# Performance work log

Hardware: AMD Instinct MI355X
Metric: run time of the kernel (lower is better)

The kernel has to match this reference:

```python
import jax, jax.numpy as jnp
import numpy as np

D = 2048
HQ = 32
HKV = 8
DH = D // HQ          # 64
GROUP = HQ // HKV     # 4
B, T = 2, 2048


def setup_inputs() -> dict:
    key = jax.random.key(0)
    ks = jax.random.split(key, 5)
    s = 0.02
    return {
        "x": jax.random.normal(ks[0], (B, T, D), dtype=jnp.float32),
        "Wq": jax.random.normal(ks[1], (D, D), dtype=jnp.float32) * s,
        "Wk": jax.random.normal(ks[2], (D, HKV * DH), dtype=jnp.float32) * s,
        "Wv": jax.random.normal(ks[3], (D, HKV * DH), dtype=jnp.float32) * s,
        "Wo": jax.random.normal(ks[4], (D, D), dtype=jnp.float32) * s,
    }


def reference(x, Wq, Wk, Wv, Wo):
    Bsz, Tlen, _ = x.shape
    # projections
    q = (x @ Wq).reshape(Bsz, Tlen, HQ, DH).transpose(0, 2, 1, 3)    # [B,hq,T,dh]
    k = (x @ Wk).reshape(Bsz, Tlen, HKV, DH).transpose(0, 2, 1, 3)   # [B,hkv,T,dh]
    v = (x @ Wv).reshape(Bsz, Tlen, HKV, DH).transpose(0, 2, 1, 3)
    # GQA: repeat each kv head GROUP times along the head dim
    k = jnp.repeat(k, GROUP, axis=1)                                  # [B,hq,T,dh]
    v = jnp.repeat(v, GROUP, axis=1)
    scale = 1.0 / jnp.sqrt(jnp.asarray(DH, dtype=x.dtype))
    att = jnp.einsum("bhqd,bhkd->bhqk", q, k) * scale                # [B,hq,T,T]
    p = jax.nn.softmax(att, axis=-1)
    out = jnp.einsum("bhqk,bhkd->bhqd", p, v)                        # [B,hq,T,dh]
    out = out.transpose(0, 2, 1, 3).reshape(Bsz, Tlen, D)            # [B,T,D]
    return out @ Wo
```

## Files before the change

### kernel.cpp

```cpp
#include <hip/hip_runtime.h>
#include <stdint.h>

typedef __bf16 bf16;
typedef __bf16 bf16x8 __attribute__((ext_vector_type(8)));
typedef __bf16 bf16x4_t __attribute__((ext_vector_type(4)));
typedef float f32x4 __attribute__((ext_vector_type(4)));

#define HQ_N 32
#define DH_N 64
#define SEQ 2048
#define NTOK 4096

#if __has_builtin(__builtin_amdgcn_exp2f)
#define EXP2(x) __builtin_amdgcn_exp2f(x)
#else
#define EXP2(x) __expf((x) * 0.69314718056f)
#endif

#define QSCALE 0.18033688011112042f

__device__ __forceinline__ void async_ld16(const bf16* g, bf16* l) {
    __builtin_amdgcn_global_load_lds(
        (__attribute__((address_space(1))) void*)(uintptr_t)(g),
        (__attribute__((address_space(3))) void*)(uint32_t)(uintptr_t)(l),
        16, 0, 0);
}

__global__ __launch_bounds__(256) void k_cast_bf16(const float* __restrict__ in,
                                                   bf16* __restrict__ out, int n4) {
    int i = blockIdx.x * 256 + threadIdx.x;
    if (i < n4) {
        float4 f = ((const float4*)in)[i];
        bf16x4_t v = {(bf16)f.x, (bf16)f.y, (bf16)f.z, (bf16)f.w};
        ((bf16x4_t*)out)[i] = v;
    }
}

__global__ __launch_bounds__(256) void k_cast_transpose(const float* __restrict__ in,
                                                        bf16* __restrict__ out,
                                                        int R, int C) {
    __shared__ float t[64][65];
    const int tid = threadIdx.x;
    const int c0 = blockIdx.x * 64, r0 = blockIdx.y * 64;
#pragma unroll
    for (int c = 0; c < 4; ++c) {
        int i = tid + c * 256;
        int row = i >> 4, cc = (i & 15) * 4;
        float4 v = *(const float4*)(in + (size_t)(r0 + row) * C + c0 + cc);
        t[row][cc + 0] = v.x; t[row][cc + 1] = v.y;
        t[row][cc + 2] = v.z; t[row][cc + 3] = v.w;
    }
    __syncthreads();
#pragma unroll
    for (int c = 0; c < 4; ++c) {
        int i = tid + c * 256;
        int row = i >> 4, cc = (i & 15) * 4;
        bf16x4_t v = {(bf16)t[cc + 0][row], (bf16)t[cc + 1][row],
                      (bf16)t[cc + 2][row], (bf16)t[cc + 3][row]};
        *(bf16x4_t*)(out + (size_t)(c0 + row) * R + r0 + cc) = v;
    }
}

__global__ __launch_bounds__(256, 3) void k_gemm(
    const bf16* __restrict__ A, const bf16* __restrict__ BT,
    int lda, int ldb, int M, int N, int K, int mode,
    float* __restrict__ Cf, int ldc,
    bf16* __restrict__ Qb, bf16* __restrict__ Kb, bf16* __restrict__ VTb)
{
    __shared__ bf16 S[16384];
    bf16* As = S;
    bf16* Bs = S + 8192;

    const int tid  = threadIdx.x;
    const int lane = tid & 63;
    const int w    = tid >> 6;
    const int l15  = lane & 15, quad = lane >> 4;
    const int l7   = l15 & 7;
    const int wm = (w >> 1) * 64, wn = (w & 1) * 64;

    const int mb = M >> 7;
    const int band = blockIdx.x / (mb * 8);
    const int rsr  = blockIdx.x % (mb * 8);
    const int mi = rsr >> 3, ni = band * 8 + (rsr & 7);

    const int srow = tid >> 3;
    const int sc8e = ((tid & 7) ^ (srow & 7)) * 8;
    const bf16* aP = A  + (size_t)(mi * 128 + srow) * lda + sc8e;
    const bf16* bP = BT + (size_t)(ni * 128 + srow) * ldb + sc8e;

    f32x4 acc[4][4] = {};

    for (int k0 = 0; k0 < K; k0 += 64) {
        __syncthreads();
#pragma unroll
        for (int c = 0; c < 4; ++c) {
            async_ld16(aP + (size_t)c * 32 * lda, &As[(tid + c * 256) * 8]);
            async_ld16(bP + (size_t)c * 32 * ldb, &Bs[(tid + c * 256) * 8]);
        }
        aP += 64; bP += 64;
        __syncthreads();
#pragma unroll
        for (int ks = 0; ks < 2; ++ks) {
            const int ch = 8 * (((ks << 2) | quad) ^ l7);
            bf16x8 af[4], bfr[4];
#pragma unroll
            for (int mt = 0; mt < 4; ++mt)
                af[mt] = *(const bf16x8*)(As + (wm + mt * 16 + l15) * 64 + ch);
#pragma unroll
            for (int nt = 0; nt < 4; ++nt)
                bfr[nt] = *(const bf16x8*)(Bs + (wn + nt * 16 + l15) * 64 + ch);
#pragma unroll
            for (int mt = 0; mt < 4; ++mt)
#pragma unroll
                for (int nt = 0; nt < 4; ++nt)
                    acc[mt][nt] = __builtin_amdgcn_mfma_f32_16x16x32_bf16(
                        af[mt], bfr[nt], acc[mt][nt], 0, 0, 0);
        }
    }

    if (mode == 2) {
#pragma unroll
        for (int mt = 0; mt < 4; ++mt)
#pragma unroll
            for (int nt = 0; nt < 4; ++nt) {
                int rg0 = mi * 128 + wm + mt * 16 + quad * 4;
                int cg  = ni * 128 + wn + nt * 16 + l15;
#pragma unroll
                for (int r = 0; r < 4; ++r)
                    Cf[(size_t)(rg0 + r) * ldc + cg] = acc[mt][nt][r];
            }
    } else if (ni < 16) {
#pragma unroll
        for (int mt = 0; mt < 4; ++mt)
#pragma unroll
            for (int nt = 0; nt < 4; ++nt) {
                int rg0 = mi * 128 + wm + mt * 16 + quad * 4;
                int cg  = ni * 128 + wn + nt * 16 + l15;
#pragma unroll
                for (int r = 0; r < 4; ++r)
                    Qb[(size_t)(rg0 + r) * 2048 + cg] = (bf16)(acc[mt][nt][r] * QSCALE);
            }
    } else if (ni < 20) {
#pragma unroll
        for (int mt = 0; mt < 4; ++mt)
#pragma unroll
            for (int nt = 0; nt < 4; ++nt) {
                int rg0 = mi * 128 + wm + mt * 16 + quad * 4;
                int cg  = ni * 128 + wn + nt * 16 + l15 - 2048;
#pragma unroll
                for (int r = 0; r < 4; ++r)
                    Kb[(size_t)(rg0 + r) * 512 + cg] = (bf16)acc[mt][nt][r];
            }
    } else {
        __syncthreads();
#pragma unroll
        for (int mt = 0; mt < 4; ++mt)
#pragma unroll
            for (int nt = 0; nt < 4; ++nt) {
                int rl0 = wm + mt * 16 + quad * 4;
                int cl  = wn + nt * 16 + l15;
#pragma unroll
                for (int r = 0; r < 4; ++r)
                    S[cl * 128 + rl0 + r] = (bf16)acc[mt][nt][r];
            }
        __syncthreads();
        const int v0 = ni * 128 - 2560;
#pragma unroll
        for (int c = 0; c < 8; ++c) {
            int i = tid + c * 256;
            int row = i >> 4, c8 = (i & 15) * 8;
            uint4 vv = *(const uint4*)(S + row * 128 + c8);
            *(uint4*)(VTb + (size_t)(v0 + row) * NTOK + mi * 128 + c8) = vv;
        }
    }
}

__global__ __launch_bounds__(256, 2) void k_attn(
    const bf16* __restrict__ Qb,
    const bf16* __restrict__ Kb,
    const bf16* __restrict__ VTb,
    bf16* __restrict__ Ob)
{
    __shared__ bf16 Ks[64 * 64];
    __shared__ bf16 Vt[64 * 64];
    __shared__ bf16 Ps[256 * 64];
    __shared__ float Ls[256];

    const int tid  = threadIdx.x;
    const int lane = tid & 63;
    const int w    = tid >> 6;
    const int l15  = lane & 15, quad = lane >> 4;
    const int l7   = l15 & 7;

    const int bid = blockIdx.x;
    const int qt  = bid & 7;
    const int hq  = (bid >> 3) & 31;
    const int b   = bid >> 8;
    const int hkv = hq >> 2;
    const int q0  = qt * 256;
    const int wq0 = w * 64;
    const size_t tokbase = (size_t)b * SEQ;

    bf16* Pw = Ps + w * (64 * 64);

    const int srow = tid >> 3;
    const int sc8e = ((tid & 7) ^ (srow & 7)) * 8;
    const bf16* kP = Kb  + (tokbase + srow) * 512 + hkv * DH_N + sc8e;
    const bf16* vP = VTb + ((size_t)hkv * DH_N + srow) * NTOK + tokbase + sc8e;

    bf16x8 qf[4][2];
#pragma unroll
    for (int nt = 0; nt < 4; ++nt)
#pragma unroll
        for (int ks = 0; ks < 2; ++ks)
            qf[nt][ks] = *(const bf16x8*)(
                Qb + (tokbase + q0 + wq0 + nt * 16 + l15) * 2048 + hq * DH_N + ks * 32 + quad * 8);

    f32x4 acc_o[4][4] = {};
    float lsum[4] = {0.f, 0.f, 0.f, 0.f};

    for (int kt = 0; kt < 32; ++kt) {
        __syncthreads();
#pragma unroll
        for (int c = 0; c < 2; ++c) {
            async_ld16(kP + (size_t)c * 32 * 512,  &Ks[(tid + c * 256) * 8]);
            async_ld16(vP + (size_t)c * 32 * NTOK, &Vt[(tid + c * 256) * 8]);
        }
        kP += 64 * 512;
        vP += 64;
        __syncthreads();

        f32x4 accs[4][4] = {};
#pragma unroll
        for (int ks = 0; ks < 2; ++ks) {
            const int ch = 8 * (((ks << 2) | quad) ^ l7);
            bf16x8 kf[4];
#pragma unroll
            for (int mt = 0; mt < 4; ++mt)
                kf[mt] = *(const bf16x8*)(Ks + (mt * 16 + l15) * 64 + ch);
#pragma unroll
            for (int mt = 0; mt < 4; ++mt)
#pragma unroll
                for (int nt = 0; nt < 4; ++nt)
                    accs[mt][nt] = __builtin_amdgcn_mfma_f32_16x16x32_bf16(
                        kf[mt], qf[nt][ks], accs[mt][nt], 0, 0, 0);
        }

#pragma unroll
        for (int mt = 0; mt < 4; ++mt) {
            const int wch = (mt * 2 + (quad >> 1));
            const int sub = (quad & 1) * 4;
#pragma unroll
            for (int nt = 0; nt < 4; ++nt) {
                float p0 = EXP2(accs[mt][nt][0]);
                float p1 = EXP2(accs[mt][nt][1]);
                float p2 = EXP2(accs[mt][nt][2]);
                float p3 = EXP2(accs[mt][nt][3]);
                lsum[nt] += (p0 + p1) + (p2 + p3);
                bf16x4_t pv = {(bf16)p0, (bf16)p1, (bf16)p2, (bf16)p3};
                *(bf16x4_t*)&Pw[(nt * 16 + l15) * 64 + 8 * (wch ^ l7) + sub] = pv;
            }
        }

#pragma unroll
        for (int ks = 0; ks < 2; ++ks) {
            const int ch = 8 * (((ks << 2) | quad) ^ l7);
            bf16x8 pf[4], vf[4];
#pragma unroll
            for (int mt = 0; mt < 4; ++mt)
                pf[mt] = *(const bf16x8*)(Pw + (mt * 16 + l15) * 64 + ch);
#pragma unroll
            for (int nt = 0; nt < 4; ++nt)
                vf[nt] = *(const bf16x8*)(Vt + (nt * 16 + l15) * 64 + ch);
#pragma unroll
            for (int mt = 0; mt < 4; ++mt)
#pragma unroll
                for (int nt = 0; nt < 4; ++nt)
                    acc_o[mt][nt] = __builtin_amdgcn_mfma_f32_16x16x32_bf16(
                        pf[mt], vf[nt], acc_o[mt][nt], 0, 0, 0);
        }
    }

#pragma unroll
    for (int nt = 0; nt < 4; ++nt) {
        float s = lsum[nt];
        s += __shfl_xor(s, 16);
        s += __shfl_xor(s, 32);
        Ls[w * 64 + nt * 16 + l15] = 1.0f / s;
    }

#pragma unroll
    for (int mt = 0; mt < 4; ++mt) {
#pragma unroll
        for (int r = 0; r < 4; ++r) {
            float rl = Ls[w * 64 + mt * 16 + quad * 4 + r];
            int qrow = q0 + wq0 + mt * 16 + quad * 4 + r;
#pragma unroll
            for (int nt = 0; nt < 4; ++nt) {
                float v = acc_o[mt][nt][r] * rl;
                Ob[(tokbase + qrow) * 2048 + hq * DH_N + nt * 16 + l15] = (bf16)v;
            }
        }
    }
}

extern "C" void kernel_launch(void* const* d_in, const int* in_sizes, int n_in,
                              void* d_out, int out_size, void* d_ws, size_t ws_size,
                              hipStream_t stream)
{
    const float* x  = (const float*)d_in[0];
    const float* Wq = (const float*)d_in[1];
    const float* Wk = (const float*)d_in[2];
    const float* Wv = (const float*)d_in[3];
    const float* Wo = (const float*)d_in[4];
    float* out = (float*)d_out;

    bf16* ws    = (bf16*)d_ws;
    bf16* xb    = ws;
    bf16* WqkvT = xb    + (size_t)4096 * 2048;
    bf16* WoT   = WqkvT + (size_t)3072 * 2048;
    bf16* Qb    = WoT   + (size_t)2048 * 2048;
    bf16* Kb    = Qb    + (size_t)4096 * 2048;
    bf16* VTb   = Kb    + (size_t)4096 * 512;
    bf16* Ob    = VTb   + (size_t)512 * 4096;

    k_cast_bf16<<<8192, 256, 0, stream>>>(x, xb, 4096 * 2048 / 4);
    k_cast_transpose<<<dim3(32, 32), 256, 0, stream>>>(Wq, WqkvT, 2048, 2048);
    k_cast_transpose<<<dim3(8, 32), 256, 0, stream>>>(Wk, WqkvT + (size_t)2048 * 2048, 2048, 512);
    k_cast_transpose<<<dim3(8, 32), 256, 0, stream>>>(Wv, WqkvT + (size_t)2560 * 2048, 2048, 512);
    k_cast_transpose<<<dim3(32, 32), 256, 0, stream>>>(Wo, WoT, 2048, 2048);

    k_gemm<<<(4096 / 128) * (3072 / 128), 256, 0, stream>>>(
        xb, WqkvT, 2048, 2048, 4096, 3072, 2048, 1,
        nullptr, 0, Qb, Kb, VTb);

    k_attn<<<512, 256, 0, stream>>>(Qb, Kb, VTb, Ob);

    k_gemm<<<(4096 / 128) * (2048 / 128), 256, 0, stream>>>(
        Ob, WoT, 2048, 2048, 4096, 2048, 2048, 2,
        out, 2048, nullptr, nullptr, nullptr);
}
```

Baseline: 302.0 us.

## Double-buffer GEMM and attention LDS tiles and merge weight cast-transpose launches

The GEMM now uses two 32-wide K stages in LDS: it prefetches the next stage asynchronously while computing the current one, with a new XOR swizzle suited to 32-column rows. It also requests occupancy 4. The attention kernel double-buffers its K/V tiles so the next tile's load overlaps the current QK/PV compute, which drops one barrier per iteration. The four weight cast-transpose launches are merged into one launch over a z-dimension, with blocks that fall outside a matrix returning early. In exchange, attention uses more LDS, which may reduce occupancy, and the smaller GEMM K step halves the work done between barriers.

```diff
diff --git a/kernel.cpp b/kernel.cpp
--- a/kernel.cpp
+++ b/kernel.cpp
@@ -36,9 +36,20 @@
     }
 }
 
-__global__ __launch_bounds__(256) void k_cast_transpose(const float* __restrict__ in,
-                                                        bf16* __restrict__ out,
-                                                        int R, int C) {
+__global__ __launch_bounds__(256) void k_cast_transpose_all(
+    const float* __restrict__ Wq, const float* __restrict__ Wk,
+    const float* __restrict__ Wv, const float* __restrict__ Wo,
+    bf16* __restrict__ WqkvT, bf16* __restrict__ WoT)
+{
+    const int z = blockIdx.z;
+    const float* in; bf16* out; int C;
+    const int R = 2048;
+    if      (z == 0) { in = Wq; out = WqkvT;                        C = 2048; }
+    else if (z == 1) { in = Wk; out = WqkvT + (size_t)2048 * 2048;  C = 512;  }
+    else if (z == 2) { in = Wv; out = WqkvT + (size_t)2560 * 2048;  C = 512;  }
+    else             { in = Wo; out = WoT;                          C = 2048; }
+    if (blockIdx.x * 64 >= C) return;
+
     __shared__ float t[64][65];
     const int tid = threadIdx.x;
     const int c0 = blockIdx.x * 64, r0 = blockIdx.y * 64;
@@ -61,21 +72,18 @@
     }
 }
 
-__global__ __launch_bounds__(256, 3) void k_gemm(
+__global__ __launch_bounds__(256, 4) void k_gemm(
     const bf16* __restrict__ A, const bf16* __restrict__ BT,
     int lda, int ldb, int M, int N, int K, int mode,
     float* __restrict__ Cf, int ldc,
     bf16* __restrict__ Qb, bf16* __restrict__ Kb, bf16* __restrict__ VTb)
 {
     __shared__ bf16 S[16384];
-    bf16* As = S;
-    bf16* Bs = S + 8192;
 
     const int tid  = threadIdx.x;
     const int lane = tid & 63;
     const int w    = tid >> 6;
     const int l15  = lane & 15, quad = lane >> 4;
-    const int l7   = l15 & 7;
     const int wm = (w >> 1) * 64, wn = (w & 1) * 64;
 
     const int mb = M >> 7;
@@ -83,39 +91,52 @@
     const int rsr  = blockIdx.x % (mb * 8);
     const int mi = rsr >> 3, ni = band * 8 + (rsr & 7);
 
-    const int srow = tid >> 3;
-    const int sc8e = ((tid & 7) ^ (srow & 7)) * 8;
-    const bf16* aP = A  + (size_t)(mi * 128 + srow) * lda + sc8e;
-    const bf16* bP = BT + (size_t)(ni * 128 + srow) * ldb + sc8e;
+    const int srow0 = tid >> 2;
+    const int lc = (tid & 3) ^ (srow0 & 3) ^ ((srow0 >> 2) & 3);
+    const bf16* aP = A  + (size_t)(mi * 128 + srow0) * lda + lc * 8;
+    const bf16* bP = BT + (size_t)(ni * 128 + srow0) * ldb + lc * 8;
+
+    const int ch = 8 * (quad ^ (l15 & 3) ^ (l15 >> 2));
 
     f32x4 acc[4][4] = {};
 
-    for (int k0 = 0; k0 < K; k0 += 64) {
+    {
+        bf16* As = S; bf16* Bs = S + 4096;
+#pragma unroll
+        for (int c = 0; c < 2; ++c) {
+            async_ld16(aP + (size_t)c * 64 * lda, &As[(tid + c * 256) * 8]);
+            async_ld16(bP + (size_t)c * 64 * ldb, &Bs[(tid + c * 256) * 8]);
+        }
+    }
+
+    int st = 0;
+    for (int k0 = 0; k0 < K; k0 += 32) {
         __syncthreads();
-#pragma unroll
-        for (int c = 0; c < 4; ++c) {
-            async_ld16(aP + (size_t)c * 32 * lda, &As[(tid + c * 256) * 8]);
-            async_ld16(bP + (size_t)c * 32 * ldb, &Bs[(tid + c * 256) * 8]);
-        }
-        aP += 64; bP += 64;
-        __syncthreads();
-#pragma unroll
-        for (int ks = 0; ks < 2; ++ks) {
-            const int ch = 8 * (((ks << 2) | quad) ^ l7);
-            bf16x8 af[4], bfr[4];
-#pragma unroll
-            for (int mt = 0; mt < 4; ++mt)
-                af[mt] = *(const bf16x8*)(As + (wm + mt * 16 + l15) * 64 + ch);
+        if (k0 + 32 < K) {
+            bf16* An = S + ((st ^ 1) << 13);
+            bf16* Bn = An + 4096;
+#pragma unroll
+            for (int c = 0; c < 2; ++c) {
+                async_ld16(aP + (k0 + 32) + (size_t)c * 64 * lda, &An[(tid + c * 256) * 8]);
+                async_ld16(bP + (k0 + 32) + (size_t)c * 64 * ldb, &Bn[(tid + c * 256) * 8]);
+            }
+        }
+        const bf16* As = S + (st << 13);
+        const bf16* Bs = As + 4096;
+        bf16x8 af[4], bfr[4];
+#pragma unroll
+        for (int mt = 0; mt < 4; ++mt)
+            af[mt] = *(const bf16x8*)(As + (wm + mt * 16 + l15) * 32 + ch);
+#pragma unroll
+        for (int nt = 0; nt < 4; ++nt)
+            bfr[nt] = *(const bf16x8*)(Bs + (wn + nt * 16 + l15) * 32 + ch);
+#pragma unroll
+        for (int mt = 0; mt < 4; ++mt)
 #pragma unroll
             for (int nt = 0; nt < 4; ++nt)
-                bfr[nt] = *(const bf16x8*)(Bs + (wn + nt * 16 + l15) * 64 + ch);
-#pragma unroll
-            for (int mt = 0; mt < 4; ++mt)
-#pragma unroll
-                for (int nt = 0; nt < 4; ++nt)
-                    acc[mt][nt] = __builtin_amdgcn_mfma_f32_16x16x32_bf16(
-                        af[mt], bfr[nt], acc[mt][nt], 0, 0, 0);
-        }
+                acc[mt][nt] = __builtin_amdgcn_mfma_f32_16x16x32_bf16(
+                    af[mt], bfr[nt], acc[mt][nt], 0, 0, 0);
+        st ^= 1;
     }
 
     if (mode == 2) {
@@ -181,8 +202,8 @@
     const bf16* __restrict__ VTb,
     bf16* __restrict__ Ob)
 {
-    __shared__ bf16 Ks[64 * 64];
-    __shared__ bf16 Vt[64 * 64];
+    __shared__ bf16 Ks[2][64 * 64];
+    __shared__ bf16 Vt[2][64 * 64];
     __shared__ bf16 Ps[256 * 64];
     __shared__ float Ls[256];
 
@@ -219,16 +240,26 @@
     f32x4 acc_o[4][4] = {};
     float lsum[4] = {0.f, 0.f, 0.f, 0.f};
 
+#pragma unroll
+    for (int c = 0; c < 2; ++c) {
+        async_ld16(kP + (size_t)c * 32 * 512,  &Ks[0][(tid + c * 256) * 8]);
+        async_ld16(vP + (size_t)c * 32 * NTOK, &Vt[0][(tid + c * 256) * 8]);
+    }
+    kP += 64 * 512;
+    vP += 64;
+
+    int st = 0;
     for (int kt = 0; kt < 32; ++kt) {
         __syncthreads();
-#pragma unroll
-        for (int c = 0; c < 2; ++c) {
-            async_ld16(kP + (size_t)c * 32 * 512,  &Ks[(tid + c * 256) * 8]);
-            async_ld16(vP + (size_t)c * 32 * NTOK, &Vt[(tid + c * 256) * 8]);
-        }
-        kP += 64 * 512;
-        vP += 64;
-        __syncthreads();
+        if (kt + 1 < 32) {
+#pragma unroll
+            for (int c = 0; c < 2; ++c) {
+                async_ld16(kP + (size_t)c * 32 * 512,  &Ks[st ^ 1][(tid + c * 256) * 8]);
+                async_ld16(vP + (size_t)c * 32 * NTOK, &Vt[st ^ 1][(tid + c * 256) * 8]);
+            }
+            kP += 64 * 512;
+            vP += 64;
+        }
 
         f32x4 accs[4][4] = {};
 #pragma unroll
@@ -237,7 +268,7 @@
             bf16x8 kf[4];
 #pragma unroll
             for (int mt = 0; mt < 4; ++mt)
-                kf[mt] = *(const bf16x8*)(Ks + (mt * 16 + l15) * 64 + ch);
+                kf[mt] = *(const bf16x8*)(&Ks[st][0] + (mt * 16 + l15) * 64 + ch);
 #pragma unroll
             for (int mt = 0; mt < 4; ++mt)
 #pragma unroll
@@ -271,7 +302,7 @@
                 pf[mt] = *(const bf16x8*)(Pw + (mt * 16 + l15) * 64 + ch);
 #pragma unroll
             for (int nt = 0; nt < 4; ++nt)
-                vf[nt] = *(const bf16x8*)(Vt + (nt * 16 + l15) * 64 + ch);
+                vf[nt] = *(const bf16x8*)(&Vt[st][0] + (nt * 16 + l15) * 64 + ch);
 #pragma unroll
             for (int mt = 0; mt < 4; ++mt)
 #pragma unroll
@@ -279,6 +310,7 @@
                     acc_o[mt][nt] = __builtin_amdgcn_mfma_f32_16x16x32_bf16(
                         pf[mt], vf[nt], acc_o[mt][nt], 0, 0, 0);
         }
+        st ^= 1;
     }
 
 #pragma unroll
@@ -325,10 +357,8 @@
     bf16* Ob    = VTb   + (size_t)512 * 4096;
 
     k_cast_bf16<<<8192, 256, 0, stream>>>(x, xb, 4096 * 2048 / 4);
-    k_cast_transpose<<<dim3(32, 32), 256, 0, stream>>>(Wq, WqkvT, 2048, 2048);
-    k_cast_transpose<<<dim3(8, 32), 256, 0, stream>>>(Wk, WqkvT + (size_t)2048 * 2048, 2048, 512);
-    k_cast_transpose<<<dim3(8, 32), 256, 0, stream>>>(Wv, WqkvT + (size_t)2560 * 2048, 2048, 512);
-    k_cast_transpose<<<dim3(32, 32), 256, 0, stream>>>(Wo, WoT, 2048, 2048);
+    k_cast_transpose_all<<<dim3(32, 32, 4), 256, 0, stream>>>(
+        Wq, Wk, Wv, Wo, WqkvT, WoT);
 
     k_gemm<<<(4096 / 128) * (3072 / 128), 256, 0, stream>>>(
         xb, WqkvT, 2048, 2048, 4096, 3072, 2048, 1,
```

Measured after the change: 307.4 us. Within noise of the previous version (+1.8%).

## Merge cast/transpose prep kernels and pad attention P tile in LDS

Applied to the files above, without the earlier changes.

Fuses the x cast and the four weight cast-transpose launches into one 3D-grid prep kernel, which cuts four kernel launches and the tail bubbles between them. In attention, the per-warp P scratch changes from an XOR-swizzled 64-wide layout to a padded 72-wide row layout, which simplifies P write and read addressing. K/V pointer arithmetic is recomputed from the tile index instead of incremented. The change adds a little LDS use and may alter the bank-conflict pattern on P accesses. Some prep blocks exit early when they fall outside the narrower K/V weights.

```diff
diff --git a/kernel.cpp b/kernel.cpp
--- a/kernel.cpp
+++ b/kernel.cpp
@@ -26,21 +26,32 @@
         16, 0, 0);
 }
 
-__global__ __launch_bounds__(256) void k_cast_bf16(const float* __restrict__ in,
-                                                   bf16* __restrict__ out, int n4) {
-    int i = blockIdx.x * 256 + threadIdx.x;
-    if (i < n4) {
-        float4 f = ((const float4*)in)[i];
+__global__ __launch_bounds__(256) void k_prep(
+    const float* __restrict__ x,
+    const float* __restrict__ Wq, const float* __restrict__ Wk,
+    const float* __restrict__ Wv, const float* __restrict__ Wo,
+    bf16* __restrict__ xb, bf16* __restrict__ WqkvT, bf16* __restrict__ WoT)
+{
+    const int z = blockIdx.z;
+    const int tid = threadIdx.x;
+
+    if (z >= 4) {
+        int i = ((z - 4) * 1024 + blockIdx.y * 32 + blockIdx.x) * 256 + tid;
+        float4 f = ((const float4*)x)[i];
         bf16x4_t v = {(bf16)f.x, (bf16)f.y, (bf16)f.z, (bf16)f.w};
-        ((bf16x4_t*)out)[i] = v;
-    }
-}
-
-__global__ __launch_bounds__(256) void k_cast_transpose(const float* __restrict__ in,
-                                                        bf16* __restrict__ out,
-                                                        int R, int C) {
+        ((bf16x4_t*)xb)[i] = v;
+        return;
+    }
+
+    const float* in; bf16* out; int C;
+    const int R = 2048;
+    if      (z == 0) { in = Wq; out = WqkvT;                        C = 2048; }
+    else if (z == 1) { in = Wk; out = WqkvT + (size_t)2048 * 2048;  C = 512;  }
+    else if (z == 2) { in = Wv; out = WqkvT + (size_t)2560 * 2048;  C = 512;  }
+    else             { in = Wo; out = WoT;                          C = 2048; }
+    if (blockIdx.x * 64 >= C) return;
+
     __shared__ float t[64][65];
-    const int tid = threadIdx.x;
     const int c0 = blockIdx.x * 64, r0 = blockIdx.y * 64;
 #pragma unroll
     for (int c = 0; c < 4; ++c) {
@@ -183,7 +194,7 @@
 {
     __shared__ bf16 Ks[64 * 64];
     __shared__ bf16 Vt[64 * 64];
-    __shared__ bf16 Ps[256 * 64];
+    __shared__ bf16 Ps[4 * 64 * 72];
     __shared__ float Ls[256];
 
     const int tid  = threadIdx.x;
@@ -201,7 +212,7 @@
     const int wq0 = w * 64;
     const size_t tokbase = (size_t)b * SEQ;
 
-    bf16* Pw = Ps + w * (64 * 64);
+    bf16* Pw = Ps + w * (64 * 72);
 
     const int srow = tid >> 3;
     const int sc8e = ((tid & 7) ^ (srow & 7)) * 8;
@@ -220,14 +231,13 @@
     float lsum[4] = {0.f, 0.f, 0.f, 0.f};
 
     for (int kt = 0; kt < 32; ++kt) {
+        const int k0 = kt * 64;
         __syncthreads();
 #pragma unroll
         for (int c = 0; c < 2; ++c) {
-            async_ld16(kP + (size_t)c * 32 * 512,  &Ks[(tid + c * 256) * 8]);
-            async_ld16(vP + (size_t)c * 32 * NTOK, &Vt[(tid + c * 256) * 8]);
-        }
-        kP += 64 * 512;
-        vP += 64;
+            async_ld16(kP + (size_t)(k0 + c * 32) * 512, &Ks[(tid + c * 256) * 8]);
+            async_ld16(vP + k0 + (size_t)c * 32 * NTOK,  &Vt[(tid + c * 256) * 8]);
+        }
         __syncthreads();
 
         f32x4 accs[4][4] = {};
@@ -248,8 +258,6 @@
 
 #pragma unroll
         for (int mt = 0; mt < 4; ++mt) {
-            const int wch = (mt * 2 + (quad >> 1));
-            const int sub = (quad & 1) * 4;
 #pragma unroll
             for (int nt = 0; nt < 4; ++nt) {
                 float p0 = EXP2(accs[mt][nt][0]);
@@ -258,20 +266,21 @@
                 float p3 = EXP2(accs[mt][nt][3]);
                 lsum[nt] += (p0 + p1) + (p2 + p3);
                 bf16x4_t pv = {(bf16)p0, (bf16)p1, (bf16)p2, (bf16)p3};
-                *(bf16x4_t*)&Pw[(nt * 16 + l15) * 64 + 8 * (wch ^ l7) + sub] = pv;
+                *(bf16x4_t*)&Pw[(nt * 16 + l15) * 72 + mt * 16 + quad * 4] = pv;
             }
         }
 
 #pragma unroll
         for (int ks = 0; ks < 2; ++ks) {
-            const int ch = 8 * (((ks << 2) | quad) ^ l7);
+            const int chv = 8 * (((ks << 2) | quad) ^ l7);
+            const int chp = ks * 32 + quad * 8;
             bf16x8 pf[4], vf[4];
 #pragma unroll
             for (int mt = 0; mt < 4; ++mt)
-                pf[mt] = *(const bf16x8*)(Pw + (mt * 16 + l15) * 64 + ch);
+                pf[mt] = *(const bf16x8*)(Pw + (mt * 16 + l15) * 72 + chp);
 #pragma unroll
             for (int nt = 0; nt < 4; ++nt)
-                vf[nt] = *(const bf16x8*)(Vt + (nt * 16 + l15) * 64 + ch);
+                vf[nt] = *(const bf16x8*)(Vt + (nt * 16 + l15) * 64 + chv);
 #pragma unroll
             for (int mt = 0; mt < 4; ++mt)
 #pragma unroll
@@ -324,11 +333,8 @@
     bf16* VTb   = Kb    + (size_t)4096 * 512;
     bf16* Ob    = VTb   + (size_t)512 * 4096;
 
-    k_cast_bf16<<<8192, 256, 0, stream>>>(x, xb, 4096 * 2048 / 4);
-    k_cast_transpose<<<dim3(32, 32), 256, 0, stream>>>(Wq, WqkvT, 2048, 2048);
-    k_cast_transpose<<<dim3(8, 32), 256, 0, stream>>>(Wk, WqkvT + (size_t)2048 * 2048, 2048, 512);
-    k_cast_transpose<<<dim3(8, 32), 256, 0, stream>>>(Wv, WqkvT + (size_t)2560 * 2048, 2048, 512);
-    k_cast_transpose<<<dim3(32, 32), 256, 0, stream>>>(Wo, WoT, 2048, 2048);
+    k_prep<<<dim3(32, 32, 12), 256, 0, stream>>>(
+        x, Wq, Wk, Wv, Wo, xb, WqkvT, WoT);
 
     k_gemm<<<(4096 / 128) * (3072 / 128), 256, 0, stream>>>(
         xb, WqkvT, 2048, 2048, 4096, 3072, 2048, 1,
```

Measured after the change: 295.3 us. 1.02x faster.
